# Optimization experiments

Measured on AMD Instinct MI355X. Metric: run time of the kernel, lower is better.

The kernel has to match this reference:

```python
import jax, jax.numpy as jnp
import numpy as np

B, T, D = 2, 1024, 1024
H, HKV = 16, 4
HD = D // H            # 64, head dim
GROUPS = H // HKV      # 4
E, K, F = 32, 4, 256   # experts, top-k, expert hidden
FS = 2 * F             # shared expert hidden = n_shared_experts * expert_dim
ROPE_THETA = 500000.0


def rmsnorm(x, w, eps=1e-6):
    return x * jax.lax.rsqrt(jnp.mean(x * x, axis=-1, keepdims=True) + eps) * w


def apply_rope(x, cos, sin):
    # x: (B, T, H, HD); pairs of adjacent features form complex numbers
    xr = x.reshape(*x.shape[:-1], -1, 2)
    a, b = xr[..., 0], xr[..., 1]
    c = cos[None, :, None, :]
    s = sin[None, :, None, :]
    out = jnp.stack([a * c - b * s, a * s + b * c], axis=-1)
    return out.reshape(x.shape)


def setup_inputs():
    key = jax.random.key(0)
    ks = jax.random.split(key, 14)
    # RoPE phasors (real/imag of freqs_cis), shape (T, HD//2)
    inv = 1.0 / (ROPE_THETA ** (np.arange(0, HD, 2, dtype=np.float32) / HD))
    ang = np.arange(T, dtype=np.float32)[:, None] * inv[None, :]
    n = lambda k, shape, d: (jax.random.normal(k, shape, jnp.float32) / np.sqrt(d))
    return {
        "x": jax.random.normal(ks[0], (B, T, D), jnp.float32),
        "freqs_cos": jnp.asarray(np.cos(ang)),
        "freqs_sin": jnp.asarray(np.sin(ang)),
        "norm1_w": jnp.ones((D,), jnp.float32),
        "norm2_w": jnp.ones((D,), jnp.float32),
        "wq": n(ks[1], (D, H * HD), D),
        "wk": n(ks[2], (D, HKV * HD), D),
        "wv": n(ks[3], (D, HKV * HD), D),
        "wo": n(ks[4], (H * HD, D), H * HD),
        "router_w": n(ks[5], (D, E), D),
        "w_gate": n(ks[6], (E, D, F), D),
        "w_up": n(ks[7], (E, D, F), D),
        "w_down": n(ks[8], (E, F, D), F),
        "sh_gate": n(ks[9], (D, FS), D),
        "sh_up": n(ks[10], (D, FS), D),
        "sh_down": n(ks[11], (FS, D), FS),
    }


def reference(x, freqs_cos, freqs_sin, norm1_w, norm2_w, wq, wk, wv, wo,
              router_w, w_gate, w_up, w_down, sh_gate, sh_up, sh_down):
    # ---- GQA attention (pre-norm, residual), eval mode, causal ----
    h = rmsnorm(x, norm1_w)
    q = (h @ wq).reshape(B, T, H, HD)
    k = (h @ wk).reshape(B, T, HKV, HD)
    v = (h @ wv).reshape(B, T, HKV, HD)
    q = apply_rope(q, freqs_cos, freqs_sin)
    k = apply_rope(k, freqs_cos, freqs_sin)
    k = jnp.repeat(k, GROUPS, axis=2)   # (B, T, H, HD)
    v = jnp.repeat(v, GROUPS, axis=2)
    scores = jnp.einsum("bqhd,bkhd->bhqk", q, k) * (HD ** -0.5)
    causal = jnp.tril(jnp.ones((T, T), bool))
    scores = jnp.where(causal[None, None], scores, jnp.finfo(scores.dtype).min)
    probs = jax.nn.softmax(scores, axis=-1)
    attn = jnp.einsum("bhqk,bkhd->bqhd", probs, v).reshape(B, T, H * HD)
    x = x + attn @ wo

    # ---- top-K routed MoE SwiGLU FFN + shared expert (pre-norm, residual) ----
    h = rmsnorm(x, norm2_w).reshape(-1, D)              # (N, D)
    gate_scores = jax.nn.softmax(h @ router_w, axis=-1) # (N, E)
    top_vals, top_idx = jax.lax.top_k(gate_scores, K)   # (N, K)
    combine = jnp.sum(jax.nn.one_hot(top_idx, E, dtype=h.dtype) * top_vals[..., None], axis=1)  # (N, E)
    g = jnp.einsum("nd,edf->nef", h, w_gate)
    u = jnp.einsum("nd,edf->nef", h, w_up)
    hh = jax.nn.silu(g) * u * combine[:, :, None]       # combine-masked: only top-K experts contribute
    routed = jnp.einsum("nef,efd->nd", hh, w_down)
    shared = (jax.nn.silu(h @ sh_gate) * (h @ sh_up)) @ sh_down
    return x + (routed + shared).reshape(B, T, D)
```

## Files before the change

kernel.cpp:

```cpp
#include <hip/hip_runtime.h>

typedef unsigned short u16;
typedef _Float16 h8v __attribute__((ext_vector_type(8)));
typedef __attribute__((ext_vector_type(4))) float f4v;

#define DEV static __device__ __forceinline__

DEV u16 f2h(float f) {
  union { _Float16 h; u16 u; } v; v.h = (_Float16)f; return v.u;
}
DEV float h2f(u16 u) {
  union { u16 u; _Float16 h; } v; v.u = u; return (float)v.h;
}

DEV f4v mfma16h(h8v a, h8v b, f4v c) {
  return __builtin_amdgcn_mfma_f32_16x16x32_f16(a, b, c, 0, 0, 0);
}

__global__ __launch_bounds__(256) void prep_kernel(
    const float* __restrict__ wq, const float* __restrict__ wk,
    const float* __restrict__ wv, const float* __restrict__ wo,
    const float* __restrict__ shg, const float* __restrict__ shu,
    const float* __restrict__ shd,
    const float* __restrict__ wg, const float* __restrict__ wu,
    const float* __restrict__ wd,
    u16* __restrict__ wqkvT, u16* __restrict__ woT, u16* __restrict__ shguT,
    u16* __restrict__ shdT, u16* __restrict__ wguT, u16* __restrict__ wdT,
    const float* __restrict__ x, const float* __restrict__ n1w,
    u16* __restrict__ hH, int* __restrict__ counts) {
  int blk = blockIdx.x;
  if (blk < 7168) {
    const float* in; u16* out; int R, C, gx, gy; long long ozs; int base;
    int rmul, radd;
    if (blk < 256)       { in=wq;  out=wqkvT;                    R=1024; C=1024; gx=16; gy=16; ozs=0;        base=0;    rmul=1; radd=0; }
    else if (blk < 320)  { in=wk;  out=wqkvT+(size_t)1024*1024;  R=1024; C=256;  gx=4;  gy=16; ozs=0;        base=256;  rmul=1; radd=0; }
    else if (blk < 384)  { in=wv;  out=wqkvT+(size_t)1280*1024;  R=1024; C=256;  gx=4;  gy=16; ozs=0;        base=320;  rmul=1; radd=0; }
    else if (blk < 640)  { in=wo;  out=woT;                      R=1024; C=1024; gx=16; gy=16; ozs=0;        base=384;  rmul=1; radd=0; }
    else if (blk < 768)  { in=shg; out=shguT;                    R=1024; C=512;  gx=8;  gy=16; ozs=0;        base=640;  rmul=2; radd=0; }
    else if (blk < 896)  { in=shu; out=shguT;                    R=1024; C=512;  gx=8;  gy=16; ozs=0;        base=768;  rmul=2; radd=1; }
    else if (blk < 1024) { in=shd; out=shdT;                     R=512;  C=1024; gx=16; gy=8;  ozs=0;        base=896;  rmul=1; radd=0; }
    else if (blk < 3072) { in=wg;  out=wguT;                     R=1024; C=256;  gx=4;  gy=16; ozs=512*1024; base=1024; rmul=2; radd=0; }
    else if (blk < 5120) { in=wu;  out=wguT;                     R=1024; C=256;  gx=4;  gy=16; ozs=512*1024; base=3072; rmul=2; radd=1; }
    else                 { in=wd;  out=wdT;                      R=256;  C=1024; gx=16; gy=4;  ozs=256*1024; base=5120; rmul=1; radd=0; }
    int i = blk - base;
    int bx = i % gx; int rem = i / gx; int by = rem % gy; int z = rem / gy;
    __shared__ float tile[64][65];
    const float* inp = in + (size_t)z * R * C;
    u16* op = out + (size_t)z * ozs;
    int c0 = bx * 64, r0 = by * 64;
    int tcol = (threadIdx.x & 15) * 4;
    int trow = threadIdx.x >> 4;
    #pragma unroll
    for (int p = 0; p < 4; ++p) {
      int row = trow + p*16;
      float4 v = *(const float4*)(inp + (size_t)(r0+row)*C + c0 + tcol);
      tile[row][tcol] = v.x; tile[row][tcol+1] = v.y;
      tile[row][tcol+2] = v.z; tile[row][tcol+3] = v.w;
    }
    __syncthreads();
    int tcol8 = (threadIdx.x & 7) * 8;
    int trow2 = threadIdx.x >> 3;
    #pragma unroll
    for (int p = 0; p < 2; ++p) {
      int c = trow2 + p*32;
      uint4 ov;
      ov.x = (unsigned)f2h(tile[tcol8+0][c]) | ((unsigned)f2h(tile[tcol8+1][c]) << 16);
      ov.y = (unsigned)f2h(tile[tcol8+2][c]) | ((unsigned)f2h(tile[tcol8+3][c]) << 16);
      ov.z = (unsigned)f2h(tile[tcol8+4][c]) | ((unsigned)f2h(tile[tcol8+5][c]) << 16);
      ov.w = (unsigned)f2h(tile[tcol8+6][c]) | ((unsigned)f2h(tile[tcol8+7][c]) << 16);
      *(uint4*)(op + (size_t)((c0+c)*rmul + radd)*R + r0 + tcol8) = ov;
    }
  } else if (blk < 9216) {
    int n = blk - 7168;
    int t = threadIdx.x;
    const float* xr = x + (size_t)n * 1024;
    float4 v = ((const float4*)xr)[t];
    float ss = v.x*v.x + v.y*v.y + v.z*v.z + v.w*v.w;
    #pragma unroll
    for (int o = 1; o < 64; o <<= 1) ss += __shfl_xor(ss, o, 64);
    __shared__ float wsum[4];
    if ((t & 63) == 0) wsum[t >> 6] = ss;
    __syncthreads();
    float tot = wsum[0] + wsum[1] + wsum[2] + wsum[3];
    float rs = rsqrtf(tot * (1.0f/1024.0f) + 1e-6f);
    float4 wv4 = ((const float4*)n1w)[t];
    ushort4 oh = { f2h(v.x*rs*wv4.x), f2h(v.y*rs*wv4.y),
                   f2h(v.z*rs*wv4.z), f2h(v.w*rs*wv4.w) };
    ((ushort4*)(hH + (size_t)n*1024))[t] = oh;
  } else {
    if (threadIdx.x < 32) counts[threadIdx.x] = 0;
  }
}

__global__ __launch_bounds__(256) void rmsnorm_kernel(const float* __restrict__ xin,
                                                      const float* __restrict__ w,
                                                      u16* __restrict__ outH,
                                                      float* __restrict__ outF) {
  int n = blockIdx.x;
  int t = threadIdx.x;
  const float* xr = xin + (size_t)n * 1024;
  float4 v = ((const float4*)xr)[t];
  float ss = v.x*v.x + v.y*v.y + v.z*v.z + v.w*v.w;
  #pragma unroll
  for (int o = 1; o < 64; o <<= 1) ss += __shfl_xor(ss, o, 64);
  __shared__ float wsum[4];
  if ((t & 63) == 0) wsum[t >> 6] = ss;
  __syncthreads();
  float tot = wsum[0] + wsum[1] + wsum[2] + wsum[3];
  float rs = rsqrtf(tot * (1.0f/1024.0f) + 1e-6f);
  float4 wv = ((const float4*)w)[t];
  float o0 = v.x*rs*wv.x, o1 = v.y*rs*wv.y, o2 = v.z*rs*wv.z, o3 = v.w*rs*wv.w;
  if (outF) {
    float4 of = {o0, o1, o2, o3};
    ((float4*)(outF + (size_t)n*1024))[t] = of;
  }
  ushort4 oh = { f2h(o0), f2h(o1), f2h(o2), f2h(o3) };
  ((ushort4*)(outH + (size_t)n*1024))[t] = oh;
}

__global__ __launch_bounds__(256) void gemm_kernel(
    const u16* __restrict__ Ah,
    const u16* __restrict__ Bh,
    float* __restrict__ C, u16* __restrict__ Ch16,
    u16* __restrict__ Csilu, const float* __restrict__ wtpP,
    u16* __restrict__ Qr, u16* __restrict__ Kr, u16* __restrict__ Vr,
    const float* __restrict__ fcP, const float* __restrict__ fsP,
    const float* __restrict__ resid,
    const int* __restrict__ rowIdx, const int* __restrict__ counts,
    const int* __restrict__ offsets,
    int M, int N, int K, int strideBTe) {
  int M_ = M;
  const int* rIdx = rowIdx;
  int aOff = 0;
  if (counts) {
    int e = blockIdx.z;
    M_ = counts[e];
    if ((int)blockIdx.y * 64 >= M_) return;
    aOff = offsets[e];
    Bh += (size_t)e * strideBTe;
    if (Csilu)      Csilu += (size_t)aOff * (N >> 1);
    else if (Ch16)  Ch16  += (size_t)aOff * N;
    else            C     += (size_t)aOff * N;
    if (wtpP) wtpP += aOff;
    if (rIdx) rIdx += aOff;
  }
  __shared__ u16 AtH[64*72];
  __shared__ u16 BtH[64*72];

  int tid = threadIdx.x;
  int wid = tid >> 6, lane = tid & 63;
  int lo16 = lane & 15, hi4 = lane >> 4;
  int m0 = blockIdx.y * 64, n0 = blockIdx.x * 64;
  int srow = tid >> 2, sseg = (tid & 3) * 16;

  int am = m0 + srow;
  int arow;
  if (counts) {
    int mm = (am < M_) ? am : (M_ - 1);
    arow = rIdx ? rIdx[mm] : (aOff + mm);
  } else {
    arow = am;
  }
  const u16* aPH = Ah + (size_t)arow * K;
  const u16* bPH = Bh + (size_t)(n0 + srow) * K;

  uint4 a0r, a1r, b0r, b1r;
  #define GLOAD(kb) { \
    a0r = *(const uint4*)(aPH + (kb) + sseg); a1r = *(const uint4*)(aPH + (kb) + sseg + 8); \
    b0r = *(const uint4*)(bPH + (kb) + sseg); b1r = *(const uint4*)(bPH + (kb) + sseg + 8); }
  #define GSTORE() { \
    *(uint4*)&AtH[srow*72 + sseg] = a0r; *(uint4*)&AtH[srow*72 + sseg + 8] = a1r; \
    *(uint4*)&BtH[srow*72 + sseg] = b0r; *(uint4*)&BtH[srow*72 + sseg + 8] = b1r; }

  f4v acc[4];
  #pragma unroll
  for (int j = 0; j < 4; ++j) { acc[j][0]=0.f; acc[j][1]=0.f; acc[j][2]=0.f; acc[j][3]=0.f; }

  GLOAD(0); GSTORE();
  for (int kb = 0; kb < K; kb += 64) {
    __syncthreads();
    if (kb + 64 < K) GLOAD(kb + 64);
    int ar = wid*16 + lo16;
    h8v ah0 = *(const h8v*)&AtH[ar*72 + 8*hi4];
    h8v ah1 = *(const h8v*)&AtH[ar*72 + 32 + 8*hi4];
    #pragma unroll
    for (int j = 0; j < 4; ++j) {
      int br = j*16 + lo16;
      h8v bh0 = *(const h8v*)&BtH[br*72 + 8*hi4];
      h8v bh1 = *(const h8v*)&BtH[br*72 + 32 + 8*hi4];
      acc[j] = mfma16h(ah0, bh0, acc[j]);
      acc[j] = mfma16h(ah1, bh1, acc[j]);
    }
    __syncthreads();
    if (kb + 64 < K) GSTORE();
  }
  #undef GLOAD
  #undef GSTORE
  #pragma unroll
  for (int r = 0; r < 4; ++r) {
    int rg = m0 + wid*16 + 4*hi4 + r;
    if (rg < M_) {
      if (Qr) {
        int b = rg >> 10, t = rg & 1023;
        #pragma unroll
        for (int j = 0; j < 4; ++j) {
          int cg = n0 + j*16 + lo16;
          float own = acc[j][r];
          float oth = __shfl_xor(own, 1, 64);
          if (cg < 1280) {
            int d = cg & 63;
            float c = fcP[t*32 + (d >> 1)];
            float s = fsP[t*32 + (d >> 1)];
            float o = ((lane & 1) == 0) ? (own*c - oth*s) : (oth*s + own*c);
            if (cg < 1024) {
              int hh = cg >> 6;
              Qr[(((size_t)(b*16 + hh))*1024 + t)*64 + d] = f2h(o);
            } else {
              int kv = (cg - 1024) >> 6;
              Kr[(((size_t)(b*4 + kv))*1024 + t)*64 + d] = f2h(o);
            }
          } else {
            int kv = (cg - 1280) >> 6;
            int hd = cg & 63;
            Vr[(((size_t)(b*4 + kv))*64 + hd)*1024 + t] = f2h(own);
          }
        }
      } else if (Csilu) {
        size_t rb = (size_t)rg * (N >> 1);
        #pragma unroll
        for (int j = 0; j < 4; ++j) {
          float own = acc[j][r];
          float oth = __shfl_xor(own, 1, 64);
          if ((lo16 & 1) == 0) {
            float sg = own / (1.f + expf(-own));
            float res = sg * oth;
            if (wtpP) res *= wtpP[rg];
            int cg = n0 + j*16 + lo16;
            Csilu[rb + (cg >> 1)] = f2h(res);
          }
        }
      } else {
        size_t rb = (size_t)rg * N;
        #pragma unroll
        for (int j = 0; j < 4; ++j) {
          int cg = n0 + j*16 + lo16;
          float v = acc[j][r];
          if (resid) v += resid[rb + cg];
          if (Ch16) Ch16[rb + cg] = f2h(v);
          else      C[rb + cg] = v;
        }
      }
    }
  }
}

__global__ __launch_bounds__(256) void attn_kernel(
    const u16* __restrict__ Qh,
    const u16* __restrict__ Kh_,
    const u16* __restrict__ Vh_,
    u16* __restrict__ Oh) {
  int b = blockIdx.z, h = blockIdx.y;
  int qb = (b == 0) ? (int)blockIdx.x : (15 - (int)blockIdx.x);
  int kv = h >> 2;
  size_t qoff = ((size_t)(b*16 + h)) * 65536;
  size_t koff = ((size_t)(b*4 + kv)) * 65536;

  __shared__ u16 KtH[64*72], VtH[64*72];
  __shared__ u16 PtH[4][16*72];

  int tid = threadIdx.x, wid = tid >> 6, lane = tid & 63;
  int lo16 = lane & 15, hi4 = lane >> 4;
  int srow = tid >> 2, sseg = (tid & 3) * 16;

  int qrow = qb*64 + wid*16 + lo16;
  const u16* qbh_ = Qh + qoff + (size_t)qrow*64;
  h8v qh0 = *(const h8v*)(qbh_ + 8*hi4);
  h8v qh1 = *(const h8v*)(qbh_ + 32 + 8*hi4);

  const u16* Kh = Kh_ + koff;
  const u16* Vh = Vh_ + koff;

  uint4 kh0r, kh1r, vh0r, vh1r;
  #define LOADT(kb) { \
    const u16* kh = Kh + (size_t)((kb)*64 + srow)*64 + sseg; \
    const u16* vh = Vh + (size_t)srow*1024 + (kb)*64 + sseg; \
    kh0r = *(const uint4*)(kh); kh1r = *(const uint4*)(kh + 8); \
    vh0r = *(const uint4*)(vh); vh1r = *(const uint4*)(vh + 8); }
  #define STORET() { \
    *(uint4*)&KtH[srow*72 + sseg]     = kh0r; *(uint4*)&KtH[srow*72 + sseg + 8] = kh1r; \
    *(uint4*)&VtH[srow*72 + sseg]     = vh0r; *(uint4*)&VtH[srow*72 + sseg + 8] = vh1r; }

  f4v oacc[4];
  #pragma unroll
  for (int j = 0; j < 4; ++j) { oacc[j][0]=0.f; oacc[j][1]=0.f; oacc[j][2]=0.f; oacc[j][3]=0.f; }
  float mrow[4] = {-1e30f, -1e30f, -1e30f, -1e30f};
  float lrow[4] = {0.f, 0.f, 0.f, 0.f};
  int qmy = qb*64 + wid*16 + 4*hi4;
  u16* PwH = PtH[wid];

  const float SC = 0.125f * 1.44269504088896f;

  LOADT(0); STORET();
  for (int kblk = 0; kblk <= qb; ++kblk) {
    __syncthreads();
    if (kblk < qb) LOADT(kblk + 1);

    f4v sfr[4];
    __builtin_amdgcn_s_setprio(1);
    #pragma unroll
    for (int j = 0; j < 4; ++j) {
      int kr = j*16 + lo16;
      h8v kh0 = *(const h8v*)&KtH[kr*72 + 8*hi4];
      h8v kh1 = *(const h8v*)&KtH[kr*72 + 32 + 8*hi4];
      f4v s; s[0]=0.f; s[1]=0.f; s[2]=0.f; s[3]=0.f;
      s = mfma16h(qh0, kh0, s);
      s = mfma16h(qh1, kh1, s);
      sfr[j] = s;
    }
    __builtin_amdgcn_s_setprio(0);

    bool diag = (kblk == qb);
    float scl[4];
    #pragma unroll
    for (int r = 0; r < 4; ++r) {
      int qr = qmy + r;
      #pragma unroll
      for (int j = 0; j < 4; ++j) {
        float v = sfr[j][r] * SC;
        if (diag) {
          int kc = kblk*64 + j*16 + lo16;
          v = (kc > qr) ? -1e30f : v;
        }
        sfr[j][r] = v;
      }
      float mx = fmaxf(fmaxf(sfr[0][r], sfr[1][r]), fmaxf(sfr[2][r], sfr[3][r]));
      #pragma unroll
      for (int o = 1; o < 16; o <<= 1) mx = fmaxf(mx, __shfl_xor(mx, o, 64));
      float mnew = fmaxf(mrow[r], mx);
      scl[r] = exp2f(mrow[r] - mnew);
      mrow[r] = mnew;
      float sum = 0.f;
      #pragma unroll
      for (int j = 0; j < 4; ++j) {
        float pv = exp2f(sfr[j][r] - mnew);
        sfr[j][r] = pv;
        sum += pv;
      }
      #pragma unroll
      for (int o = 1; o < 16; o <<= 1) sum += __shfl_xor(sum, o, 64);
      lrow[r] = lrow[r] * scl[r] + sum;
    }
    #pragma unroll
    for (int j = 0; j < 4; ++j) {
      #pragma unroll
      for (int r = 0; r < 4; ++r) oacc[j][r] *= scl[r];
    }

    #pragma unroll
    for (int r = 0; r < 4; ++r) {
      #pragma unroll
      for (int j = 0; j < 4; ++j) {
        PwH[(4*hi4 + r)*72 + j*16 + lo16] = f2h(sfr[j][r]);
      }
    }
    asm volatile("s_waitcnt lgkmcnt(0)" ::: "memory");
    h8v ph0 = *(const h8v*)&PwH[lo16*72 + 8*hi4];
    h8v ph1 = *(const h8v*)&PwH[lo16*72 + 32 + 8*hi4];

    __builtin_amdgcn_s_setprio(1);
    #pragma unroll
    for (int j = 0; j < 4; ++j) {
      int vr = j*16 + lo16;
      h8v vh0 = *(const h8v*)&VtH[vr*72 + 8*hi4];
      h8v vh1 = *(const h8v*)&VtH[vr*72 + 32 + 8*hi4];
      oacc[j] = mfma16h(ph0, vh0, oacc[j]);
      oacc[j] = mfma16h(ph1, vh1, oacc[j]);
    }
    __builtin_amdgcn_s_setprio(0);

    __syncthreads();
    if (kblk < qb) STORET();
  }
  #undef LOADT
  #undef STORET

  #pragma unroll
  for (int r = 0; r < 4; ++r) {
    float inv = 1.f / lrow[r];
    int tq = qb*64 + wid*16 + 4*hi4 + r;
    size_t base = ((size_t)(b*1024 + tq))*1024 + h*64;
    #pragma unroll
    for (int j = 0; j < 4; ++j) {
      Oh[base + j*16 + lo16] = f2h(oacc[j][r] * inv);
    }
  }
}

__global__ __launch_bounds__(256) void router_kernel(const float* __restrict__ h2,
                                                     const float* __restrict__ rw,
                                                     int* __restrict__ topIdx, float* __restrict__ topW,
                                                     int* __restrict__ counts) {
  __shared__ float hs[2][1024];
  __shared__ float part[4][32];
  __shared__ int hist[32];
  int t = threadIdx.x;
  int row0 = blockIdx.x * 2;
  if (t < 32) hist[t] = 0;

  {
    const float4* hsrc = (const float4*)(h2 + (size_t)row0 * 1024);
    float4* hdst = (float4*)&hs[0][0];
    hdst[t] = hsrc[t];
    hdst[t + 256] = hsrc[t + 256];
  }
  __syncthreads();

  int e = t & 31, g = t >> 5;
  int r = g >> 2, q = g & 3;
  const float* hp = &hs[r][q*256];
  const float* rp = rw + (size_t)(q*256)*32 + e;
  float b0 = 0.f, b1 = 0.f, b2 = 0.f, b3 = 0.f;
  #pragma unroll 16
  for (int d = 0; d < 256; d += 4) {
    b0 += hp[d+0] * rp[(d+0)*32];
    b1 += hp[d+1] * rp[(d+1)*32];
    b2 += hp[d+2] * rp[(d+2)*32];
    b3 += hp[d+3] * rp[(d+3)*32];
  }
  float pq = (b0 + b1) + (b2 + b3);
  pq += __shfl_xor(pq, 32, 64);
  int w = t >> 6;
  if ((t & 63) < 32) part[w][e] = pq;
  __syncthreads();

  if ((w & 1) == 0 && (t & 63) < 32) {
    float lg = part[w][e] + part[w+1][e];
    float mx = lg;
    #pragma unroll
    for (int o = 1; o < 32; o <<= 1) mx = fmaxf(mx, __shfl_xor(mx, o, 64));
    float ex = expf(lg - mx);
    float sm = ex;
    #pragma unroll
    for (int o = 1; o < 32; o <<= 1) sm += __shfl_xor(sm, o, 64);
    float prob = ex / sm;

    float pv = prob; int pi = e;
    int myRow = row0 + (w >> 1);
    for (int k = 0; k < 4; ++k) {
      float bv = pv; int bi = pi;
      #pragma unroll
      for (int o = 1; o < 32; o <<= 1) {
        float ov = __shfl_xor(bv, o, 64); int oi = __shfl_xor(bi, o, 64);
        if (ov > bv || (ov == bv && oi < bi)) { bv = ov; bi = oi; }
      }
      if (e == 0) {
        topIdx[myRow*4 + k] = bi; topW[myRow*4 + k] = bv;
        atomicAdd(&hist[bi], 1);
      }
      if (pi == bi) pv = -1.f;
    }
  }
  __syncthreads();
  if (t < 32 && hist[t] > 0) atomicAdd(&counts[t], hist[t]);
}

__global__ __launch_bounds__(256) void scan_scatter_kernel(
    const int* __restrict__ counts, int* __restrict__ offsets,
    const int* __restrict__ topIdx, const float* __restrict__ topW,
    int* __restrict__ rows, float* __restrict__ wtp, int* __restrict__ pslot) {
  __shared__ int cur[32];
  int t = threadIdx.x;
  if (t == 0) {
    int acc = 0;
    for (int e = 0; e < 32; ++e) { offsets[e] = acc; cur[e] = acc; acc += counts[e]; }
    offsets[32] = acc;
  }
  __syncthreads();
  for (int i = t; i < 8192; i += 256) {
    int e = topIdx[i];
    int slot = atomicAdd(&cur[e], 1);
    rows[slot] = i >> 2;
    wtp[slot] = topW[i];
    pslot[i] = slot;
  }
}

__global__ __launch_bounds__(256) void final_kernel(const float* __restrict__ x1, const u16* __restrict__ shOut,
                                                    const u16* __restrict__ pairOut, const int* __restrict__ pslot,
                                                    float* __restrict__ out) {
  int n = blockIdx.x;
  int t = threadIdx.x;
  int s0 = pslot[n*4], s1 = pslot[n*4+1], s2 = pslot[n*4+2], s3 = pslot[n*4+3];
  float4 a  = ((const float4*)(x1 + (size_t)n*1024))[t];
  ushort4 sh = ((const ushort4*)(shOut + (size_t)n*1024))[t];
  ushort4 p0 = ((const ushort4*)(pairOut + (size_t)s0*1024))[t];
  ushort4 p1 = ((const ushort4*)(pairOut + (size_t)s1*1024))[t];
  ushort4 p2 = ((const ushort4*)(pairOut + (size_t)s2*1024))[t];
  ushort4 p3 = ((const ushort4*)(pairOut + (size_t)s3*1024))[t];
  float4 o;
  o.x = a.x + h2f(sh.x) + h2f(p0.x) + h2f(p1.x) + h2f(p2.x) + h2f(p3.x);
  o.y = a.y + h2f(sh.y) + h2f(p0.y) + h2f(p1.y) + h2f(p2.y) + h2f(p3.y);
  o.z = a.z + h2f(sh.z) + h2f(p0.z) + h2f(p1.z) + h2f(p2.z) + h2f(p3.z);
  o.w = a.w + h2f(sh.w) + h2f(p0.w) + h2f(p1.w) + h2f(p2.w) + h2f(p3.w);
  ((float4*)(out + (size_t)n*1024))[t] = o;
}

extern "C" void kernel_launch(void* const* d_in, const int* in_sizes, int n_in,
                              void* d_out, int out_size, void* d_ws, size_t ws_size,
                              hipStream_t stream) {
  const float* x   = (const float*)d_in[0];
  const float* fc  = (const float*)d_in[1];
  const float* fs  = (const float*)d_in[2];
  const float* n1w = (const float*)d_in[3];
  const float* n2w = (const float*)d_in[4];
  const float* wq  = (const float*)d_in[5];
  const float* wk  = (const float*)d_in[6];
  const float* wv  = (const float*)d_in[7];
  const float* wo  = (const float*)d_in[8];
  const float* rw  = (const float*)d_in[9];
  const float* wg  = (const float*)d_in[10];
  const float* wu  = (const float*)d_in[11];
  const float* wd  = (const float*)d_in[12];
  const float* shg = (const float*)d_in[13];
  const float* shu = (const float*)d_in[14];
  const float* shd = (const float*)d_in[15];
  float* out = (float*)d_out;
  (void)in_sizes; (void)n_in; (void)out_size;

  char* p = (char*)d_ws;
  auto alloc = [&](size_t n) { char* r = p; p += (n + 255) & ~(size_t)255; return r; };

  u16* wqkvT  = (u16*)alloc((size_t)1536*1024*2);
  u16* woT    = (u16*)alloc((size_t)1024*1024*2);
  u16* shguT  = (u16*)alloc((size_t)1024*1024*2);
  u16* shdT   = (u16*)alloc((size_t)1024*512*2);
  u16* wguT   = (u16*)alloc((size_t)32*512*1024*2);
  u16* wdT    = (u16*)alloc((size_t)32*1024*256*2);
  u16* hH     = (u16*)alloc((size_t)2048*1024*2);
  float* x1   = (float*)alloc((size_t)2048*1024*4);
  float* h2f_ = (float*)alloc((size_t)2048*1024*4);
  u16* h2b    = (u16*)alloc((size_t)2048*1024*2);
  u16* actb   = (u16*)alloc((size_t)8192*256*2);
  u16* sactb  = (u16*)alloc((size_t)2048*512*2);
  u16* shOut  = (u16*)alloc((size_t)2048*1024*2);
  int* topIdx = (int*)alloc(2048*4*4);
  float* topW = (float*)alloc(2048*4*4);
  int* counts = (int*)alloc(32*4);
  int* offsets = (int*)alloc(33*4);
  int* rows   = (int*)alloc(8192*4);
  float* wtp  = (float*)alloc(8192*4);
  int* pslot  = (int*)alloc(8192*4);
  char* regionStart = p;
  u16* qbh = (u16*)alloc((size_t)2048*1024*2);
  u16* kbh = (u16*)alloc((size_t)524288*2);
  u16* vth = (u16*)alloc((size_t)524288*2);
  u16* attnH = (u16*)alloc((size_t)2048*1024*2);
  u16* pairOut = (u16*)regionStart;
  {
    size_t regionBytes = (size_t)8192*1024*2;
    if ((size_t)(p - regionStart) < regionBytes) p = regionStart + regionBytes;
  }

  size_t needed = (size_t)(p - (char*)d_ws);
  if (needed > ws_size) return;

  dim3 blk(256);
  prep_kernel<<<9217, blk, 0, stream>>>(
      wq, wk, wv, wo, shg, shu, shd, wg, wu, wd,
      wqkvT, woT, shguT, shdT, wguT, wdT,
      x, n1w, hH, counts);
  gemm_kernel<<<dim3(24, 32), blk, 0, stream>>>(hH, wqkvT, nullptr, nullptr, nullptr, nullptr,
      qbh, kbh, vth, fc, fs,
      nullptr, nullptr, nullptr, nullptr, 2048, 1536, 1024, 0);
  attn_kernel<<<dim3(16,16,2), blk, 0, stream>>>(qbh, kbh, vth, attnH);
  gemm_kernel<<<dim3(16, 32), blk, 0, stream>>>(attnH, woT, x1, nullptr, nullptr, nullptr,
      nullptr, nullptr, nullptr, nullptr, nullptr,
      x, nullptr, nullptr, nullptr, 2048, 1024, 1024, 0);
  rmsnorm_kernel<<<2048, blk, 0, stream>>>(x1, n2w, h2b, h2f_);
  router_kernel<<<1024, blk, 0, stream>>>(h2f_, rw, topIdx, topW, counts);
  scan_scatter_kernel<<<1, blk, 0, stream>>>(counts, offsets, topIdx, topW, rows, wtp, pslot);
  gemm_kernel<<<dim3(16, 32), blk, 0, stream>>>(h2b, shguT, nullptr, nullptr, sactb, nullptr,
      nullptr, nullptr, nullptr, nullptr, nullptr,
      nullptr, nullptr, nullptr, nullptr, 2048, 1024, 1024, 0);
  gemm_kernel<<<dim3(16, 32), blk, 0, stream>>>(sactb, shdT, nullptr, shOut, nullptr, nullptr,
      nullptr, nullptr, nullptr, nullptr, nullptr,
      nullptr, nullptr, nullptr, nullptr, 2048, 1024, 512, 0);
  gemm_kernel<<<dim3(8, 32, 32), blk, 0, stream>>>(h2b, wguT, nullptr, nullptr, actb, wtp,
      nullptr, nullptr, nullptr, nullptr, nullptr,
      nullptr, rows, counts, offsets, 0, 512, 1024, 512*1024);
  gemm_kernel<<<dim3(16, 32, 32), blk, 0, stream>>>(actb, wdT, nullptr, pairOut, nullptr, nullptr,
      nullptr, nullptr, nullptr, nullptr, nullptr,
      nullptr, nullptr, counts, offsets, 0, 1024, 256, 1024*256);
  final_kernel<<<2048, blk, 0, stream>>>(x1, shOut, pairOut, pslot, out);
}
```

Before: 239.0 us.

## Overlap remaining weight transposes with attention in one fused launch

Splits the prep kernel so only the QKV weight transpose and first RMSNorm run before the QKV GEMM. The wo, shared-expert and routed-expert weight transposes move into extra blocks of the attention launch, letting memory-bound conversion run alongside compute-bound attention on otherwise idle CUs. The shared memory becomes one union buffer sized for both roles, which may raise LDS use per attention block and affect how its blocks are scheduled.

```diff
diff --git a/kernel.cpp b/kernel.cpp
--- a/kernel.cpp
+++ b/kernel.cpp
@@ -17,61 +17,54 @@
   return __builtin_amdgcn_mfma_f32_16x16x32_f16(a, b, c, 0, 0, 0);
 }
 
-__global__ __launch_bounds__(256) void prep_kernel(
+DEV void transpose_tile(const float* in, u16* out, int R, int C,
+                        int bx, int by, int z, long long ozs,
+                        int rmul, int radd, float (*tile)[65]) {
+  const float* inp = in + (size_t)z * R * C;
+  u16* op = out + (size_t)z * ozs;
+  int c0 = bx * 64, r0 = by * 64;
+  int tcol = (threadIdx.x & 15) * 4;
+  int trow = threadIdx.x >> 4;
+  #pragma unroll
+  for (int p = 0; p < 4; ++p) {
+    int row = trow + p*16;
+    float4 v = *(const float4*)(inp + (size_t)(r0+row)*C + c0 + tcol);
+    tile[row][tcol] = v.x; tile[row][tcol+1] = v.y;
+    tile[row][tcol+2] = v.z; tile[row][tcol+3] = v.w;
+  }
+  __syncthreads();
+  int tcol8 = (threadIdx.x & 7) * 8;
+  int trow2 = threadIdx.x >> 3;
+  #pragma unroll
+  for (int p = 0; p < 2; ++p) {
+    int c = trow2 + p*32;
+    uint4 ov;
+    ov.x = (unsigned)f2h(tile[tcol8+0][c]) | ((unsigned)f2h(tile[tcol8+1][c]) << 16);
+    ov.y = (unsigned)f2h(tile[tcol8+2][c]) | ((unsigned)f2h(tile[tcol8+3][c]) << 16);
+    ov.z = (unsigned)f2h(tile[tcol8+4][c]) | ((unsigned)f2h(tile[tcol8+5][c]) << 16);
+    ov.w = (unsigned)f2h(tile[tcol8+6][c]) | ((unsigned)f2h(tile[tcol8+7][c]) << 16);
+    *(uint4*)(op + (size_t)((c0+c)*rmul + radd)*R + r0 + tcol8) = ov;
+  }
+}
+
+__global__ __launch_bounds__(256) void prep1_kernel(
     const float* __restrict__ wq, const float* __restrict__ wk,
-    const float* __restrict__ wv, const float* __restrict__ wo,
-    const float* __restrict__ shg, const float* __restrict__ shu,
-    const float* __restrict__ shd,
-    const float* __restrict__ wg, const float* __restrict__ wu,
-    const float* __restrict__ wd,
-    u16* __restrict__ wqkvT, u16* __restrict__ woT, u16* __restrict__ shguT,
-    u16* __restrict__ shdT, u16* __restrict__ wguT, u16* __restrict__ wdT,
+    const float* __restrict__ wv,
+    u16* __restrict__ wqkvT,
     const float* __restrict__ x, const float* __restrict__ n1w,
     u16* __restrict__ hH, int* __restrict__ counts) {
   int blk = blockIdx.x;
-  if (blk < 7168) {
-    const float* in; u16* out; int R, C, gx, gy; long long ozs; int base;
-    int rmul, radd;
-    if (blk < 256)       { in=wq;  out=wqkvT;                    R=1024; C=1024; gx=16; gy=16; ozs=0;        base=0;    rmul=1; radd=0; }
-    else if (blk < 320)  { in=wk;  out=wqkvT+(size_t)1024*1024;  R=1024; C=256;  gx=4;  gy=16; ozs=0;        base=256;  rmul=1; radd=0; }
-    else if (blk < 384)  { in=wv;  out=wqkvT+(size_t)1280*1024;  R=1024; C=256;  gx=4;  gy=16; ozs=0;        base=320;  rmul=1; radd=0; }
-    else if (blk < 640)  { in=wo;  out=woT;                      R=1024; C=1024; gx=16; gy=16; ozs=0;        base=384;  rmul=1; radd=0; }
-    else if (blk < 768)  { in=shg; out=shguT;                    R=1024; C=512;  gx=8;  gy=16; ozs=0;        base=640;  rmul=2; radd=0; }
-    else if (blk < 896)  { in=shu; out=shguT;                    R=1024; C=512;  gx=8;  gy=16; ozs=0;        base=768;  rmul=2; radd=1; }
-    else if (blk < 1024) { in=shd; out=shdT;                     R=512;  C=1024; gx=16; gy=8;  ozs=0;        base=896;  rmul=1; radd=0; }
-    else if (blk < 3072) { in=wg;  out=wguT;                     R=1024; C=256;  gx=4;  gy=16; ozs=512*1024; base=1024; rmul=2; radd=0; }
-    else if (blk < 5120) { in=wu;  out=wguT;                     R=1024; C=256;  gx=4;  gy=16; ozs=512*1024; base=3072; rmul=2; radd=1; }
-    else                 { in=wd;  out=wdT;                      R=256;  C=1024; gx=16; gy=4;  ozs=256*1024; base=5120; rmul=1; radd=0; }
+  if (blk < 384) {
+    const float* in; u16* out; int R, C, gx, gy; int base;
+    if (blk < 256)      { in=wq; out=wqkvT;                   R=1024; C=1024; gx=16; gy=16; base=0; }
+    else if (blk < 320) { in=wk; out=wqkvT+(size_t)1024*1024; R=1024; C=256;  gx=4;  gy=16; base=256; }
+    else                { in=wv; out=wqkvT+(size_t)1280*1024; R=1024; C=256;  gx=4;  gy=16; base=320; }
     int i = blk - base;
     int bx = i % gx; int rem = i / gx; int by = rem % gy; int z = rem / gy;
     __shared__ float tile[64][65];
-    const float* inp = in + (size_t)z * R * C;
-    u16* op = out + (size_t)z * ozs;
-    int c0 = bx * 64, r0 = by * 64;
-    int tcol = (threadIdx.x & 15) * 4;
-    int trow = threadIdx.x >> 4;
-    #pragma unroll
-    for (int p = 0; p < 4; ++p) {
-      int row = trow + p*16;
-      float4 v = *(const float4*)(inp + (size_t)(r0+row)*C + c0 + tcol);
-      tile[row][tcol] = v.x; tile[row][tcol+1] = v.y;
-      tile[row][tcol+2] = v.z; tile[row][tcol+3] = v.w;
-    }
-    __syncthreads();
-    int tcol8 = (threadIdx.x & 7) * 8;
-    int trow2 = threadIdx.x >> 3;
-    #pragma unroll
-    for (int p = 0; p < 2; ++p) {
-      int c = trow2 + p*32;
-      uint4 ov;
-      ov.x = (unsigned)f2h(tile[tcol8+0][c]) | ((unsigned)f2h(tile[tcol8+1][c]) << 16);
-      ov.y = (unsigned)f2h(tile[tcol8+2][c]) | ((unsigned)f2h(tile[tcol8+3][c]) << 16);
-      ov.z = (unsigned)f2h(tile[tcol8+4][c]) | ((unsigned)f2h(tile[tcol8+5][c]) << 16);
-      ov.w = (unsigned)f2h(tile[tcol8+6][c]) | ((unsigned)f2h(tile[tcol8+7][c]) << 16);
-      *(uint4*)(op + (size_t)((c0+c)*rmul + radd)*R + r0 + tcol8) = ov;
-    }
-  } else if (blk < 9216) {
-    int n = blk - 7168;
+    transpose_tile(in, out, R, C, bx, by, z, 0, 1, 0, tile);
+  } else if (blk < 2432) {
+    int n = blk - 384;
     int t = threadIdx.x;
     const float* xr = x + (size_t)n * 1024;
     float4 v = ((const float4*)xr)[t];
@@ -254,19 +247,45 @@
   }
 }
 
-__global__ __launch_bounds__(256) void attn_kernel(
+__global__ __launch_bounds__(256) void attn_prep2_kernel(
     const u16* __restrict__ Qh,
     const u16* __restrict__ Kh_,
     const u16* __restrict__ Vh_,
-    u16* __restrict__ Oh) {
-  int b = blockIdx.z, h = blockIdx.y;
-  int qb = (b == 0) ? (int)blockIdx.x : (15 - (int)blockIdx.x);
+    u16* __restrict__ Oh,
+    const float* __restrict__ wo, const float* __restrict__ shg,
+    const float* __restrict__ shu, const float* __restrict__ shd,
+    const float* __restrict__ wg, const float* __restrict__ wu,
+    const float* __restrict__ wd,
+    u16* __restrict__ woT, u16* __restrict__ shguT, u16* __restrict__ shdT,
+    u16* __restrict__ wguT, u16* __restrict__ wdT) {
+  __shared__ float smemF[6912];
+  int blk = blockIdx.x;
+  if (blk >= 512) {
+    int t = blk - 512;
+    const float* in; u16* out; int R, C, gx, gy; long long ozs; int base;
+    int rmul, radd;
+    if (t < 256)       { in=wo;  out=woT;   R=1024; C=1024; gx=16; gy=16; ozs=0;        base=0;    rmul=1; radd=0; }
+    else if (t < 384)  { in=shg; out=shguT; R=1024; C=512;  gx=8;  gy=16; ozs=0;        base=256;  rmul=2; radd=0; }
+    else if (t < 512)  { in=shu; out=shguT; R=1024; C=512;  gx=8;  gy=16; ozs=0;        base=384;  rmul=2; radd=1; }
+    else if (t < 640)  { in=shd; out=shdT;  R=512;  C=1024; gx=16; gy=8;  ozs=0;        base=512;  rmul=1; radd=0; }
+    else if (t < 2688) { in=wg;  out=wguT;  R=1024; C=256;  gx=4;  gy=16; ozs=512*1024; base=640;  rmul=2; radd=0; }
+    else if (t < 4736) { in=wu;  out=wguT;  R=1024; C=256;  gx=4;  gy=16; ozs=512*1024; base=2688; rmul=2; radd=1; }
+    else               { in=wd;  out=wdT;   R=256;  C=1024; gx=16; gy=4;  ozs=256*1024; base=4736; rmul=1; radd=0; }
+    int i = t - base;
+    int bx = i % gx; int rem = i / gx; int by = rem % gy; int z = rem / gy;
+    transpose_tile(in, out, R, C, bx, by, z, ozs, rmul, radd,
+                   (float(*)[65])smemF);
+    return;
+  }
+  int xq = blk & 15, h = (blk >> 4) & 15, b = blk >> 8;
+  int qb = (b == 0) ? xq : (15 - xq);
   int kv = h >> 2;
   size_t qoff = ((size_t)(b*16 + h)) * 65536;
   size_t koff = ((size_t)(b*4 + kv)) * 65536;
 
-  __shared__ u16 KtH[64*72], VtH[64*72];
-  __shared__ u16 PtH[4][16*72];
+  u16* KtH = (u16*)smemF;
+  u16* VtH = (u16*)smemF + 4608;
+  u16* PtH = (u16*)smemF + 9216;
 
   int tid = threadIdx.x, wid = tid >> 6, lane = tid & 63;
   int lo16 = lane & 15, hi4 = lane >> 4;
@@ -296,7 +315,7 @@
   float mrow[4] = {-1e30f, -1e30f, -1e30f, -1e30f};
   float lrow[4] = {0.f, 0.f, 0.f, 0.f};
   int qmy = qb*64 + wid*16 + 4*hi4;
-  u16* PwH = PtH[wid];
+  u16* PwH = PtH + wid*1152;
 
   const float SC = 0.125f * 1.44269504088896f;
 
@@ -565,14 +584,13 @@
   if (needed > ws_size) return;
 
   dim3 blk(256);
-  prep_kernel<<<9217, blk, 0, stream>>>(
-      wq, wk, wv, wo, shg, shu, shd, wg, wu, wd,
-      wqkvT, woT, shguT, shdT, wguT, wdT,
-      x, n1w, hH, counts);
+  prep1_kernel<<<2433, blk, 0, stream>>>(wq, wk, wv, wqkvT, x, n1w, hH, counts);
   gemm_kernel<<<dim3(24, 32), blk, 0, stream>>>(hH, wqkvT, nullptr, nullptr, nullptr, nullptr,
       qbh, kbh, vth, fc, fs,
       nullptr, nullptr, nullptr, nullptr, 2048, 1536, 1024, 0);
-  attn_kernel<<<dim3(16,16,2), blk, 0, stream>>>(qbh, kbh, vth, attnH);
+  attn_prep2_kernel<<<7296, blk, 0, stream>>>(qbh, kbh, vth, attnH,
+      wo, shg, shu, shd, wg, wu, wd,
+      woT, shguT, shdT, wguT, wdT);
   gemm_kernel<<<dim3(16, 32), blk, 0, stream>>>(attnH, woT, x1, nullptr, nullptr, nullptr,
       nullptr, nullptr, nullptr, nullptr, nullptr,
       x, nullptr, nullptr, nullptr, 2048, 1024, 1024, 0);
```

Measured after the change: 221.1 us (median of 2 runs). 7.5% less time.
